# Kernel optimization log

Hardware: AMD Instinct MI355X
Metric: run time of the kernel (lower is better)

The kernel has to match this reference:

```python
import jax, jax.numpy as jnp
import numpy as np

B, O, GRID = 2048, 48, 112
SIGMA = 5.0


def setup_inputs() -> dict:
    key = jax.random.key(0)
    k1, k2, k3, k4, k5 = jax.random.split(key, 5)
    s = float(GRID - 1)
    xL = jax.random.uniform(k1, (B,), dtype=jnp.float32) * s
    yL = jax.random.uniform(k2, (B,), dtype=jnp.float32) * s
    obj_list = jax.random.uniform(k3, (B, O, 2), dtype=jnp.float32) * s
    obj_num = jax.random.randint(k4, (B,), 0, O + 1, dtype=jnp.int32)
    road_mask = jax.random.randint(k5, (B, GRID, GRID), 0, 2, dtype=jnp.int32)
    return {"xL": xL, "yL": yL, "obj_list": obj_list, "obj_num": obj_num,
            "road_mask": road_mask, "H": GRID, "W": GRID}


def reference(xL, yL, obj_list, obj_num, road_mask, H, W):
    # Faithful vectorization of batch_gaussian_tensor_obj.
    # exp(-(dx^2+dy^2)/(2s^2)) is separable: exp(-dx^2/..) * exp(-dy^2/..),
    # so per-object splats reduce to a batched matmul over the object axis.
    inv = 1.0 / (2.0 * SIGMA * SIGMA)
    x = jnp.arange(H, dtype=jnp.float32)  # row coordinate grid
    y = jnp.arange(W, dtype=jnp.float32)  # col coordinate grid

    # positive goal gaussian, rank-1 outer product per batch element
    gx = jnp.exp(-((x[None, :] - xL[:, None]) ** 2) * inv)  # [B,H]
    gy = jnp.exp(-((y[None, :] - yL[:, None]) ** 2) * inv)  # [B,W]
    goal = gx[:, :, None] * gy[:, None, :]                   # [B,H,W]

    # negative object gaussians; note original swaps xy: xo=xy[1], yo=xy[0]
    xo = obj_list[:, :, 1]  # [B,O] row coords
    yo = obj_list[:, :, 0]  # [B,O] col coords
    ex = jnp.exp(-((x[None, None, :] - xo[:, :, None]) ** 2) * inv)  # [B,O,H]
    ey = jnp.exp(-((y[None, None, :] - yo[:, :, None]) ** 2) * inv)  # [B,O,W]
    valid = (jnp.arange(O)[None, :] < obj_num[:, None]).astype(jnp.float32)  # [B,O]
    obj = jnp.einsum('boh,bow->bhw', ex * valid[:, :, None], ey)     # [B,H,W]

    channel = 0.5 + 0.5 * goal - 0.5 * obj
    channel = jnp.where(road_mask == 0, 0.0, channel)
    return channel
```

## Files before the change

### kernel.cpp

```cpp
#include <hip/hip_runtime.h>

#define GRID_N 112
#define O_MAX 48
#define HW_N (GRID_N * GRID_N)
#define NT 448
#define NB 2

typedef _Float16 half8 __attribute__((ext_vector_type(8)));
typedef float    f32x4 __attribute__((ext_vector_type(4)));
typedef float    f32x2 __attribute__((ext_vector_type(2)));

constexpr float INV = 1.0f / (2.0f * 5.0f * 5.0f);

__device__ __forceinline__ void gather_oc(const float* __restrict__ ob, int n, int quad,
                                          f32x2* oc0, f32x2* oc1) {
    #pragma unroll
    for (int j = 0; j < 8; ++j) {
        int k = quad * 8 + j;
        oc0[j] = *(const f32x2*)&ob[k * 2];
        bool g = (k + 32 < n);
        f32x2 z = {0.f, 0.f};
        oc1[j] = g ? *(const f32x2*)&ob[(k + 32) * 2] : z;
    }
}

__device__ __forceinline__ void load_masks(const int* __restrict__ rm, int h0, int m,
                                           int (*mk)[4]) {
    #pragma unroll
    for (int i = 0; i < 7; ++i) {
        int base = h0 * GRID_N + i * 16 + m;
        #pragma unroll
        for (int r = 0; r < 4; ++r)
            mk[i][r] = rm[base + r * GRID_N];
    }
}

__device__ __forceinline__ void build_a(int n, int ksteps, float fh, float xl, int quad,
                                        const f32x2* oc0, const f32x2* oc1,
                                        half8& a0, half8& a1) {
    #pragma unroll
    for (int j = 0; j < 8; ++j) {
        int k = quad * 8 + j;
        float val = 0.f;
        if (k <= n) {
            float cx = (k < n) ? oc0[j][1] : xl;
            float s  = (k < n) ? -0.5f  : 0.5f;
            float d  = fh - cx;
            val = s * __expf(-d * d * INV);
        }
        a0[j] = (_Float16)val;
    }
    if (ksteps == 2) {
        #pragma unroll
        for (int j = 0; j < 8; ++j) {
            int k = quad * 8 + j + 32;
            float val = 0.f;
            if (k <= n) {
                float cx = (k < n) ? oc1[j][1] : xl;
                float s  = (k < n) ? -0.5f  : 0.5f;
                float d  = fh - cx;
                val = s * __expf(-d * d * INV);
            }
            a1[j] = (_Float16)val;
        }
    }
}

__device__ __forceinline__ void sweep(int n, int ksteps, float yl, int m, int quad, int h0,
                                      const f32x2* oc0, const f32x2* oc1,
                                      half8 a0, half8 a1, const int (*mk)[4],
                                      float* __restrict__ op) {
    #pragma unroll
    for (int tw = 0; tw < 7; ++tw) {
        const float fw = (float)(tw * 16 + m);
        half8 b0;
        #pragma unroll
        for (int j = 0; j < 8; ++j) {
            int k = quad * 8 + j;
            float val = 0.f;
            if (k <= n) {
                float cy = (k < n) ? oc0[j][0] : yl;
                float d  = fw - cy;
                val = __expf(-d * d * INV);
            }
            b0[j] = (_Float16)val;
        }
        f32x4 acc = {0.f, 0.f, 0.f, 0.f};
        acc = __builtin_amdgcn_mfma_f32_16x16x32_f16(a0, b0, acc, 0, 0, 0);
        if (ksteps == 2) {
            half8 b1;
            #pragma unroll
            for (int j = 0; j < 8; ++j) {
                int k = quad * 8 + j + 32;
                float val = 0.f;
                if (k <= n) {
                    float cy = (k < n) ? oc1[j][0] : yl;
                    float d  = fw - cy;
                    val = __expf(-d * d * INV);
                }
                b1[j] = (_Float16)val;
            }
            acc = __builtin_amdgcn_mfma_f32_16x16x32_f16(a1, b1, acc, 0, 0, 0);
        }
        const int w0 = tw * 16 + m;
        #pragma unroll
        for (int r = 0; r < 4; ++r) {
            float v = 0.5f + acc[r];
            v = (mk[tw][r] == 0) ? 0.f : v;
            op[(h0 + r) * GRID_N + w0] = v;
        }
    }
}

__global__ __launch_bounds__(NT) void goalmap_kernel(
    const float* __restrict__ xL, const float* __restrict__ yL,
    const float* __restrict__ obj_list, const int* __restrict__ obj_num,
    const int* __restrict__ road_mask, float* __restrict__ out, int B)
{
    const int tid  = threadIdx.x;
    const int lane = tid & 63;
    const int wid  = tid >> 6;
    const int m    = lane & 15;
    const int quad = lane >> 4;
    const int h0   = wid * 16 + quad * 4;
    const float fh = (float)(wid * 16 + m);

    const int b0 = blockIdx.x * NB;
    const int b1 = b0 + 1;

    const int   n0  = obj_num[b0];
    const float xl0 = xL[b0], yl0 = yL[b0];
    const int ksteps0 = (n0 >= 32) ? 2 : 1;

    f32x2 oc0_b0[8], oc1_b0[8];
    gather_oc(obj_list + (size_t)b0 * (O_MAX * 2), n0, quad, oc0_b0, oc1_b0);
    __builtin_amdgcn_sched_barrier(0);

    int mk0[7][4];
    load_masks(road_mask + (size_t)b0 * HW_N, h0, m, mk0);
    __builtin_amdgcn_sched_barrier(0);

    f32x2 oc0_b1[8], oc1_b1[8];
    int n1 = 0; float xl1 = 0.f, yl1 = 0.f;
    const bool has_b1 = (b1 < B);
    if (has_b1) {
        n1 = obj_num[b1]; xl1 = xL[b1]; yl1 = yL[b1];
        gather_oc(obj_list + (size_t)b1 * (O_MAX * 2), n1, quad, oc0_b1, oc1_b1);
    }
    __builtin_amdgcn_sched_barrier(0);

    half8 a0_b0, a1_b0;
    build_a(n0, ksteps0, fh, xl0, quad, oc0_b0, oc1_b0, a0_b0, a1_b0);
    __builtin_amdgcn_sched_barrier(0);

    sweep(n0, ksteps0, yl0, m, quad, h0, oc0_b0, oc1_b0, a0_b0, a1_b0, mk0,
          out + (size_t)b0 * HW_N);
    __builtin_amdgcn_sched_barrier(0);

    if (has_b1) {
        const int ksteps1 = (n1 >= 32) ? 2 : 1;

        int mk1[7][4];
        load_masks(road_mask + (size_t)b1 * HW_N, h0, m, mk1);
        __builtin_amdgcn_sched_barrier(0);

        half8 a0_b1, a1_b1;
        build_a(n1, ksteps1, fh, xl1, quad, oc0_b1, oc1_b1, a0_b1, a1_b1);
        __builtin_amdgcn_sched_barrier(0);

        sweep(n1, ksteps1, yl1, m, quad, h0, oc0_b1, oc1_b1, a0_b1, a1_b1, mk1,
              out + (size_t)b1 * HW_N);
    }
}

extern "C" void kernel_launch(void* const* d_in, const int* in_sizes, int n_in,
                              void* d_out, int out_size, void* d_ws, size_t ws_size,
                              hipStream_t stream) {
    const float* xL        = (const float*)d_in[0];
    const float* yL        = (const float*)d_in[1];
    const float* obj_list  = (const float*)d_in[2];
    const int*   obj_num   = (const int*)d_in[3];
    const int*   road_mask = (const int*)d_in[4];
    float*       out       = (float*)d_out;
    const int B = in_sizes[0];

    const int grid = (B + NB - 1) / NB;
    goalmap_kernel<<<grid, NT, 0, stream>>>(xL, yL, obj_list, obj_num, road_mask, out, B);
}
```

Measured before the change: 210.6 us.

## Software-pipeline four batch items per block with double-buffered prefetch

Each block now handles four batch elements instead of two. The object coordinates and road mask for the next element are prefetched into a second register buffer while the current element is computed and stored. The object gather no longer depends on obj_num and always loads all 48 slots. This is meant to hide global load latency behind the MFMA and exp work, at the cost of more register pressure, a smaller grid (512 blocks), and less wave-level parallelism for hiding latency.

```diff
diff --git a/kernel.cpp b/kernel.cpp
--- a/kernel.cpp
+++ b/kernel.cpp
@@ -4,7 +4,7 @@
 #define O_MAX 48
 #define HW_N (GRID_N * GRID_N)
 #define NT 448
-#define NB 2
+#define NB 4
 
 typedef _Float16 half8 __attribute__((ext_vector_type(8)));
 typedef float    f32x4 __attribute__((ext_vector_type(4)));
@@ -12,15 +12,14 @@
 
 constexpr float INV = 1.0f / (2.0f * 5.0f * 5.0f);
 
-__device__ __forceinline__ void gather_oc(const float* __restrict__ ob, int n, int quad,
+__device__ __forceinline__ void gather_oc(const float* __restrict__ ob, int quad,
                                           f32x2* oc0, f32x2* oc1) {
     #pragma unroll
     for (int j = 0; j < 8; ++j) {
         int k = quad * 8 + j;
         oc0[j] = *(const f32x2*)&ob[k * 2];
-        bool g = (k + 32 < n);
         f32x2 z = {0.f, 0.f};
-        oc1[j] = g ? *(const f32x2*)&ob[(k + 32) * 2] : z;
+        oc1[j] = (k + 32 < O_MAX) ? *(const f32x2*)&ob[(k + 32) * 2] : z;
     }
 }
 
@@ -126,50 +125,48 @@
     const float fh = (float)(wid * 16 + m);
 
     const int b0 = blockIdx.x * NB;
-    const int b1 = b0 + 1;
 
-    const int   n0  = obj_num[b0];
-    const float xl0 = xL[b0], yl0 = yL[b0];
-    const int ksteps0 = (n0 >= 32) ? 2 : 1;
+    f32x2 oc0[2][8], oc1[2][8];
+    int   mk[2][7][4];
+    int   nS[2]; float xlS[2], ylS[2];
 
-    f32x2 oc0_b0[8], oc1_b0[8];
-    gather_oc(obj_list + (size_t)b0 * (O_MAX * 2), n0, quad, oc0_b0, oc1_b0);
-    __builtin_amdgcn_sched_barrier(0);
-
-    int mk0[7][4];
-    load_masks(road_mask + (size_t)b0 * HW_N, h0, m, mk0);
-    __builtin_amdgcn_sched_barrier(0);
-
-    f32x2 oc0_b1[8], oc1_b1[8];
-    int n1 = 0; float xl1 = 0.f, yl1 = 0.f;
-    const bool has_b1 = (b1 < B);
-    if (has_b1) {
-        n1 = obj_num[b1]; xl1 = xL[b1]; yl1 = yL[b1];
-        gather_oc(obj_list + (size_t)b1 * (O_MAX * 2), n1, quad, oc0_b1, oc1_b1);
+    {
+        nS[0] = obj_num[b0]; xlS[0] = xL[b0]; ylS[0] = yL[b0];
+        gather_oc(obj_list + (size_t)b0 * (O_MAX * 2), quad, oc0[0], oc1[0]);
+        __builtin_amdgcn_sched_barrier(0);
+        load_masks(road_mask + (size_t)b0 * HW_N, h0, m, mk[0]);
     }
     __builtin_amdgcn_sched_barrier(0);
 
-    half8 a0_b0, a1_b0;
-    build_a(n0, ksteps0, fh, xl0, quad, oc0_b0, oc1_b0, a0_b0, a1_b0);
-    __builtin_amdgcn_sched_barrier(0);
+    #pragma unroll
+    for (int j = 0; j < NB; ++j) {
+        const int cur = j & 1;
+        const int nxt = cur ^ 1;
+        const int bj  = b0 + j;
 
-    sweep(n0, ksteps0, yl0, m, quad, h0, oc0_b0, oc1_b0, a0_b0, a1_b0, mk0,
-          out + (size_t)b0 * HW_N);
-    __builtin_amdgcn_sched_barrier(0);
-
-    if (has_b1) {
-        const int ksteps1 = (n1 >= 32) ? 2 : 1;
-
-        int mk1[7][4];
-        load_masks(road_mask + (size_t)b1 * HW_N, h0, m, mk1);
+        if (j + 1 < NB) {
+            const int bn = b0 + j + 1;
+            if (bn < B) {
+                nS[nxt] = obj_num[bn]; xlS[nxt] = xL[bn]; ylS[nxt] = yL[bn];
+                gather_oc(obj_list + (size_t)bn * (O_MAX * 2), quad,
+                          oc0[nxt], oc1[nxt]);
+                __builtin_amdgcn_sched_barrier(0);
+                load_masks(road_mask + (size_t)bn * HW_N, h0, m, mk[nxt]);
+            }
+        }
         __builtin_amdgcn_sched_barrier(0);
 
-        half8 a0_b1, a1_b1;
-        build_a(n1, ksteps1, fh, xl1, quad, oc0_b1, oc1_b1, a0_b1, a1_b1);
+        if (bj < B) {
+            const int   n  = nS[cur];
+            const float xl = xlS[cur], yl = ylS[cur];
+            const int ksteps = (n >= 32) ? 2 : 1;
+
+            half8 a0, a1;
+            build_a(n, ksteps, fh, xl, quad, oc0[cur], oc1[cur], a0, a1);
+            sweep(n, ksteps, yl, m, quad, h0, oc0[cur], oc1[cur], a0, a1,
+                  mk[cur], out + (size_t)bj * HW_N);
+        }
         __builtin_amdgcn_sched_barrier(0);
-
-        sweep(n1, ksteps1, yl1, m, quad, h0, oc0_b1, oc1_b1, a0_b1, a1_b1, mk1,
-              out + (size_t)b1 * HW_N);
     }
 }
 
```

After: 217.2 us. 3.1% more time.
